# Performance work log

Hardware: AMD Instinct MI355X
Metric: run time of the kernel (lower is better)

Reference implementation:

```python
import jax, jax.numpy as jnp
import numpy as np

EPS = 1e-8
NUM_HEADS = 8


def setup_inputs() -> dict:
    key = jax.random.key(0)
    ks = jax.random.split(key, 12)
    B, T, F = 8, 512, 512
    H = NUM_HEADS
    dh = F // H
    maxlen = 2048
    s = 0.02  # weight init scale
    inp = {
        "x": jax.random.normal(ks[0], (B, T, F), jnp.float32),
        "Wq": jax.random.normal(ks[1], (F, F), jnp.float32) * s,
        "bq": jax.random.normal(ks[2], (F,), jnp.float32) * s,
        "Wk": jax.random.normal(ks[3], (F, F), jnp.float32) * s,
        "bk": jax.random.normal(ks[4], (F,), jnp.float32) * s,
        "Wv": jax.random.normal(ks[5], (F, F), jnp.float32) * s,
        "bv": jax.random.normal(ks[6], (F,), jnp.float32) * s,
        "Wo": jax.random.normal(ks[7], (F, F), jnp.float32) * s,
        "bo": jax.random.normal(ks[8], (F,), jnp.float32) * s,
        "delta": jnp.ones((1,), jnp.float32),
        "cache_k": jax.random.normal(ks[9], (B * H, maxlen, dh), jnp.float32) * 0.1,
        "cache_v": jax.random.normal(ks[10], (B * H, maxlen, dh), jnp.float32) * 0.1,
    }
    return inp


def _split_heads(t, H):
    # torch.cat(torch.split(t, dh, dim=-1), dim=0): head index outermost on dim 0
    B, T, F = t.shape
    dh = F // H
    return t.reshape(B, T, H, dh).transpose(2, 0, 1, 3).reshape(H * B, T, dh)


def _merge_heads(t, H):
    HB, T, dh = t.shape
    B = HB // H
    return t.reshape(H, B, T, dh).transpose(1, 2, 0, 3).reshape(B, T, H * dh)


def reference(x, Wq, bq, Wk, bk, Wv, bv, Wo, bo, delta, cache_k, cache_v):
    B, T, F = x.shape
    H = NUM_HEADS
    maxlen = cache_k.shape[1]
    d = jnp.sqrt(jnp.asarray(F, jnp.float32))

    q = _split_heads(x @ Wq.T + bq, H)  # [H*B, T, dh]
    k = _split_heads(x @ Wk.T + bk, H)
    v = _split_heads(x @ Wv.T + bv, H)

    # rolling KV cache: drop oldest T, append new T -> length maxlen
    k_full = jnp.concatenate([cache_k[:, T:], k], axis=1)  # [H*B, maxlen, dh]
    v_full = jnp.concatenate([cache_v[:, T:], v], axis=1)

    # Gaussian positional bias G = exp(-(i-j)^2 / (delta^2 + EPS)), last T rows
    i = jnp.arange(maxlen, dtype=jnp.float32)
    ind = -(i[:, None] - i[None, :]) ** 2  # [maxlen, maxlen]
    G = jnp.exp(ind[-T:] / (delta[0] ** 2 + EPS))  # [T, maxlen]

    scores = jnp.abs(jnp.einsum('btd,bsd->bts', q, k_full) * G / d)
    attn = jax.nn.softmax(scores, axis=-1)  # [H*B, T, maxlen]
    o = jnp.einsum('bts,bsd->btd', attn, v_full)  # [H*B, T, dh]

    out = _merge_heads(o, H) @ Wo.T + bo  # [B, T, F]
    return out
```

## Files before the change

### kernel.cpp

```cpp
#include <hip/hip_runtime.h>
#include <cstdint>
#include <cstddef>


typedef _Float16 f16x8 __attribute__((ext_vector_type(8)));
typedef _Float16 f16x4 __attribute__((ext_vector_type(4)));
typedef float f32x4 __attribute__((ext_vector_type(4)));

#define GLOBAL_AS __attribute__((address_space(1)))
#define LDS_AS __attribute__((address_space(3)))

__launch_bounds__(256)
__global__ void prep(const float* __restrict__ x,
                     const float* __restrict__ Wq, const float* __restrict__ Wk,
                     const float* __restrict__ Wv, const float* __restrict__ Wo,
                     const float* __restrict__ cache_v,
                     _Float16* __restrict__ xh, _Float16* __restrict__ wh,
                     float* __restrict__ part, float* __restrict__ svnew) {
  const int bid = blockIdx.x;
  const int tid = threadIdx.x;
  if (bid < 2048) {
    long e = ((long)bid * 256 + tid) * 4;
    float4 v = *(const float4*)(x + e);
    f16x4 h;
    h[0] = (_Float16)v.x; h[1] = (_Float16)v.y;
    h[2] = (_Float16)v.z; h[3] = (_Float16)v.w;
    *(f16x4*)(xh + e) = h;
  } else if (bid < 3072) {
    long e = ((long)(bid - 2048) * 256 + tid) * 4;
    int seg = (int)(e >> 18);
    const float* w = seg == 0 ? Wq : seg == 1 ? Wk : seg == 2 ? Wv : Wo;
    float4 v = *(const float4*)(w + (e & 262143));
    f16x4 h;
    h[0] = (_Float16)v.x; h[1] = (_Float16)v.y;
    h[2] = (_Float16)v.z; h[3] = (_Float16)v.w;
    *(f16x4*)(wh + e) = h;
  } else if (bid < 4096) {
    int pb = bid - 3072;
    int hb = pb >> 4, chunk = pb & 15;
    int g = tid & 15, p = tid >> 4;
    int r0 = 512 + chunk * 96;
    float4 s4 = {0.f, 0.f, 0.f, 0.f};
#pragma unroll
    for (int it = 0; it < 6; it++) {
      int r = r0 + p + it * 16;
      float4 v = *(const float4*)(cache_v + ((size_t)hb * 2048 + r) * 64 + g * 4);
      s4.x += v.x; s4.y += v.y; s4.z += v.z; s4.w += v.w;
    }
    __shared__ float4 red4[256];
    red4[tid] = s4;
    __syncthreads();
    if (tid < 64) {
      int gg = tid >> 2, c = tid & 3;
      float s = 0.f;
#pragma unroll
      for (int p2 = 0; p2 < 16; p2++) {
        float4 v = red4[p2 * 16 + gg];
        s += (c == 0) ? v.x : (c == 1) ? v.y : (c == 2) ? v.z : v.w;
      }
      part[(hb * 16 + chunk) * 64 + tid] = s;
    }
  } else {
    for (int i = tid; i < 4096; i += 256) svnew[i] = 0.f;
  }
}

__launch_bounds__(256)
__global__ void gemm_qkv(const _Float16* __restrict__ xh,
                         const _Float16* __restrict__ wh,
                         const float* __restrict__ bq,
                         const float* __restrict__ bk,
                         const float* __restrict__ bv,
                         _Float16* __restrict__ q, _Float16* __restrict__ k,
                         _Float16* __restrict__ v,
                         float* __restrict__ svnew) {
  __shared__ __align__(16) _Float16 As[4 * 128 * 32];
  __shared__ __align__(16) _Float16 Bs[4 * 64 * 32];
  const int tid = threadIdx.x;
  const int bid = blockIdx.x;
  const int swz = (bid & 7) * 96 + (bid >> 3);
  const int bx = swz / 24;
  const int by = swz - bx * 24;
  const int m0 = bx * 128;
  const int n0g = by * 64;
  const int which = n0g >> 9;
  const int nloc0 = n0g & 511;
  const _Float16* Bsel = wh + (size_t)which * 262144;
  const float* bsel = which == 0 ? bq : which == 1 ? bk : bv;
  _Float16* osel = which == 0 ? q : which == 1 ? k : v;
  const int w = tid >> 6, lane = tid & 63;
  const int c16 = lane & 15, q4 = lane >> 4;
  const int wm = (w & 1) * 64, wn = (w >> 1) * 32;

  f32x4 acc[4][2];
#pragma unroll
  for (int i = 0; i < 4; i++)
#pragma unroll
    for (int j = 0; j < 2; j++) acc[i][j] = (f32x4){0.f, 0.f, 0.f, 0.f};

  for (int k0 = 0; k0 < 512; k0 += 128) {
    __syncthreads();
#pragma unroll
    for (int it = 0; it < 8; it++) {
      int c = it * 256 + tid;
      int sub = c >> 9, row = (c >> 2) & 127, c8 = (c & 3) * 8;
      __builtin_amdgcn_global_load_lds(
          (const GLOBAL_AS void*)(xh + (size_t)(m0 + row) * 512 + k0 + sub * 32 + c8),
          (LDS_AS void*)(As + c * 8), 16, 0, 0);
    }
#pragma unroll
    for (int it = 0; it < 4; it++) {
      int c = it * 256 + tid;
      int sub = c >> 8, row = (c >> 2) & 63, c8 = (c & 3) * 8;
      __builtin_amdgcn_global_load_lds(
          (const GLOBAL_AS void*)(Bsel + (size_t)(nloc0 + row) * 512 + k0 + sub * 32 + c8),
          (LDS_AS void*)(Bs + c * 8), 16, 0, 0);
    }
    __syncthreads();

#pragma unroll
    for (int sub = 0; sub < 4; sub++) {
      f16x8 af[4], bf[2];
#pragma unroll
      for (int i = 0; i < 4; i++)
        af[i] = *(const f16x8*)(As + sub * 4096 + (wm + i * 16 + c16) * 32 + q4 * 8);
#pragma unroll
      for (int j = 0; j < 2; j++)
        bf[j] = *(const f16x8*)(Bs + sub * 2048 + (wn + j * 16 + c16) * 32 + q4 * 8);
#pragma unroll
      for (int i = 0; i < 4; i++)
#pragma unroll
        for (int j = 0; j < 2; j++)
          acc[i][j] = __builtin_amdgcn_mfma_f32_16x16x32_f16(af[i], bf[j], acc[i][j], 0, 0, 0);
    }
  }

  const int mbase = m0 + wm + (q4 << 2);
  const int nbase = nloc0 + wn + c16;
  float cs[2] = {0.f, 0.f};
#pragma unroll
  for (int i = 0; i < 4; i++)
#pragma unroll
    for (int j = 0; j < 2; j++) {
      int fg = nbase + j * 16;
      float bv2 = bsel[fg];
      int h = fg >> 6, dd = fg & 63;
#pragma unroll
      for (int r = 0; r < 4; r++) {
        int m = mbase + i * 16 + r;
        int b = m >> 9, t = m & 511;
        float val = acc[i][j][r] + bv2;
        osel[(((size_t)((h << 3) + b) * 512 + t) << 6) + dd] = (_Float16)val;
        cs[j] += val;
      }
    }
  if (which == 2) {
    const int b = m0 >> 9;
#pragma unroll
    for (int j = 0; j < 2; j++) {
      cs[j] += __shfl_xor(cs[j], 16, 64);
      cs[j] += __shfl_xor(cs[j], 32, 64);
      if (q4 == 0) {
        int fg = nbase + j * 16;
        int h = fg >> 6, dd = fg & 63;
        atomicAdd(&svnew[((h << 3) + b) * 64 + dd], cs[j]);
      }
    }
  }
}

__launch_bounds__(256)
__global__ void attn_mfma(const _Float16* __restrict__ q,
                          const _Float16* __restrict__ k_new,
                          const _Float16* __restrict__ v_new,
                          const float* __restrict__ cache_k,
                          const float* __restrict__ cache_v,
                          const float* __restrict__ part,
                          const float* __restrict__ svnew,
                          const float* __restrict__ delta,
                          _Float16* __restrict__ o_merged) {
  const int lin = blockIdx.y * 8 + blockIdx.x;
  const int swz = (lin & 7) * 64 + (lin >> 3);
  const int hb = swz >> 3;
  const int t0 = (swz & 7) * 64;
  const int jlo_t = 1520 + t0;

  __shared__ __align__(16) _Float16 Q_sh[64 * 72];
  __shared__ __align__(16) _Float16 K_sh[96 * 72];
  __shared__ __align__(16) _Float16 VT_sh[64 * 104];
  __shared__ __align__(16) _Float16 P_sh[64 * 104];
  __shared__ float G_sh[40];
  __shared__ float em_sh[64], id_sh[64], sv_sh[64];

  const int tid = threadIdx.x;
  const int w = tid >> 6, lane = tid & 63;
  const float dscale = 0.044194173824159216f;

  if (tid < 36) {
    int di = tid - 16;
    float inv_g = 1.0f / (delta[0] * delta[0] + 1e-8f);
    G_sh[tid] = (tid <= 32) ? expf(-(float)(di * di) * inv_g) : 0.f;
  }
  if (tid >= 64 && tid < 128) {
    int d = tid - 64;
    float s = svnew[hb * 64 + d];
#pragma unroll
    for (int c = 0; c < 16; c++) s += part[(hb * 16 + c) * 64 + d];
    sv_sh[d] = s;
  }
#pragma unroll
  for (int it = 0; it < 2; it++) {
    int idx = it * 256 + tid;
    int r = idx >> 3, c8 = (idx & 7) * 8;
    *(f16x8*)(Q_sh + r * 72 + c8) =
        *(const f16x8*)(q + ((size_t)hb * 512 + t0 + r) * 64 + c8);
  }
#pragma unroll
  for (int it = 0; it < 6; it++) {
    int idx = it * 256 + tid;
    int r = idx >> 4, c4 = idx & 15;
    int j = jlo_t + r;
    f16x4 kh, vh;
    if (j < 1536) {
      float4 k4 = *(const float4*)(cache_k + ((size_t)hb * 2048 + j + 512) * 64 + c4 * 4);
      float4 v4 = *(const float4*)(cache_v + ((size_t)hb * 2048 + j + 512) * 64 + c4 * 4);
      kh[0] = (_Float16)k4.x; kh[1] = (_Float16)k4.y;
      kh[2] = (_Float16)k4.z; kh[3] = (_Float16)k4.w;
      vh[0] = (_Float16)v4.x; vh[1] = (_Float16)v4.y;
      vh[2] = (_Float16)v4.z; vh[3] = (_Float16)v4.w;
    } else if (j < 2048) {
      kh = *(const f16x4*)(k_new + ((size_t)hb * 512 + (j - 1536)) * 64 + c4 * 4);
      vh = *(const f16x4*)(v_new + ((size_t)hb * 512 + (j - 1536)) * 64 + c4 * 4);
    } else {
#pragma unroll
      for (int e = 0; e < 4; e++) { kh[e] = (_Float16)0.f; vh[e] = (_Float16)0.f; }
    }
    *(f16x4*)(K_sh + r * 72 + c4 * 4) = kh;
#pragma unroll
    for (int e = 0; e < 4; e++) VT_sh[(c4 * 4 + e) * 104 + r] = vh[e];
  }
  __syncthreads();

  {
    const int c16 = lane & 15;
    const int q4 = lane >> 4;
    const int koff = q4 * 8;
    const int mrow = w * 16 + c16;
    f16x8 aq0 = *(const f16x8*)(Q_sh + mrow * 72 + koff);
    f16x8 aq1 = *(const f16x8*)(Q_sh + mrow * 72 + 32 + koff);
    f32x4 accS[6];
#pragma unroll
    for (int n = 0; n < 6; n++) accS[n] = (f32x4){0.f, 0.f, 0.f, 0.f};
    __builtin_amdgcn_s_setprio(1);
#pragma unroll
    for (int n = 0; n < 6; n++) {
      f16x8 b0 = *(const f16x8*)(K_sh + (n * 16 + c16) * 72 + koff);
      f16x8 b1 = *(const f16x8*)(K_sh + (n * 16 + c16) * 72 + 32 + koff);
      accS[n] = __builtin_amdgcn_mfma_f32_16x16x32_f16(aq0, b0, accS[n], 0, 0, 0);
      accS[n] = __builtin_amdgcn_mfma_f32_16x16x32_f16(aq1, b1, accS[n], 0, 0, 0);
    }
    __builtin_amdgcn_s_setprio(0);
    const int jmax = 527 - t0;
    float sc[6][4];
    float m_r[4] = {0.f, 0.f, 0.f, 0.f};
#pragma unroll
    for (int n = 0; n < 6; n++) {
      int jb = n * 16 + c16;
#pragma unroll
      for (int r = 0; r < 4; r++) {
        int row = w * 16 + q4 * 4 + r;
        int off = jb - row;
        bool valid = (off >= 0) && (off <= 32) && (jb <= jmax);
        int offc = min(max(off, 0), 32);
        float g = G_sh[offc];
        float val = valid ? fabsf(accS[n][r]) * dscale * g : 0.f;
        sc[n][r] = val;
        m_r[r] = fmaxf(m_r[r], val);
      }
    }
#pragma unroll
    for (int r = 0; r < 4; r++) {
#pragma unroll
      for (int mk = 1; mk < 16; mk <<= 1)
        m_r[r] = fmaxf(m_r[r], __shfl_xor(m_r[r], mk, 64));
    }
    float em_r[4], sum_r[4];
#pragma unroll
    for (int r = 0; r < 4; r++) { em_r[r] = expf(-m_r[r]); sum_r[r] = 0.f; }
#pragma unroll
    for (int n = 0; n < 6; n++) {
      int jb = n * 16 + c16;
#pragma unroll
      for (int r = 0; r < 4; r++) {
        int row = w * 16 + q4 * 4 + r;
        int off = jb - row;
        bool valid = (off >= 0) && (off <= 32) && (jb <= jmax);
        float wgt = valid ? (expf(sc[n][r] - m_r[r]) - em_r[r]) : 0.f;
        sum_r[r] += wgt;
        P_sh[row * 104 + jb] = (_Float16)wgt;
      }
    }
#pragma unroll
    for (int r = 0; r < 4; r++) {
#pragma unroll
      for (int mk = 1; mk < 16; mk <<= 1)
        sum_r[r] += __shfl_xor(sum_r[r], mk, 64);
      if (c16 == 0) {
        int row = w * 16 + q4 * 4 + r;
        em_sh[row] = em_r[r];
        id_sh[row] = 1.0f / (sum_r[r] + 2048.f * em_r[r]);
      }
    }
  }
  __syncthreads();

  f32x4 accO[4];
#pragma unroll
  for (int mi = 0; mi < 4; mi++) accO[mi] = (f32x4){0.f, 0.f, 0.f, 0.f};
  {
    const int koff = (lane >> 4) * 8;
    const int nrow = w * 16 + (lane & 15);
    __builtin_amdgcn_s_setprio(1);
#pragma unroll
    for (int k = 0; k < 3; k++) {
      f16x8 bv = *(const f16x8*)(VT_sh + nrow * 104 + k * 32 + koff);
#pragma unroll
      for (int mi = 0; mi < 4; mi++) {
        f16x8 ap = *(const f16x8*)(P_sh + (mi * 16 + (lane & 15)) * 104 + k * 32 + koff);
        accO[mi] = __builtin_amdgcn_mfma_f32_16x16x32_f16(ap, bv, accO[mi], 0, 0, 0);
      }
    }
    __builtin_amdgcn_s_setprio(0);
  }

  const int h = hb >> 3, b = hb & 7;
  const int d = w * 16 + (lane & 15);
  const float svd = sv_sh[d];
#pragma unroll
  for (int mi = 0; mi < 4; mi++)
#pragma unroll
    for (int r = 0; r < 4; r++) {
      int trow = mi * 16 + ((lane >> 4) << 2) + r;
      float val = (accO[mi][r] + em_sh[trow] * svd) * id_sh[trow];
      o_merged[((size_t)(b * 512 + t0 + trow)) * 512 + h * 64 + d] = (_Float16)val;
    }
}

__launch_bounds__(256)
__global__ void gemm_out(const _Float16* __restrict__ A,
                         const _Float16* __restrict__ Bw,
                         const float* __restrict__ bias,
                         float* __restrict__ out) {
  __shared__ __align__(16) _Float16 As[4 * 64 * 32];
  __shared__ __align__(16) _Float16 Bs[4 * 64 * 32];
  const int tid = threadIdx.x;
  const int bid = blockIdx.x;
  const int swz = (bid & 7) * 64 + (bid >> 3);
  const int m0 = (swz >> 3) * 64;
  const int n0 = (swz & 7) * 64;
  const int w = tid >> 6, lane = tid & 63;
  const int c16 = lane & 15, q4 = lane >> 4;
  const int wm = (w & 1) * 32, wn = (w >> 1) * 32;

  f32x4 acc[2][2];
#pragma unroll
  for (int i = 0; i < 2; i++)
#pragma unroll
    for (int j = 0; j < 2; j++) acc[i][j] = (f32x4){0.f, 0.f, 0.f, 0.f};

  for (int k0 = 0; k0 < 512; k0 += 128) {
    __syncthreads();
#pragma unroll
    for (int it = 0; it < 4; it++) {
      int c = it * 256 + tid;
      int sub = c >> 8, row = (c >> 2) & 63, c8 = (c & 3) * 8;
      __builtin_amdgcn_global_load_lds(
          (const GLOBAL_AS void*)(A + (size_t)(m0 + row) * 512 + k0 + sub * 32 + c8),
          (LDS_AS void*)(As + c * 8), 16, 0, 0);
      __builtin_amdgcn_global_load_lds(
          (const GLOBAL_AS void*)(Bw + (size_t)(n0 + row) * 512 + k0 + sub * 32 + c8),
          (LDS_AS void*)(Bs + c * 8), 16, 0, 0);
    }
    __syncthreads();

#pragma unroll
    for (int sub = 0; sub < 4; sub++) {
      f16x8 af[2], bf[2];
#pragma unroll
      for (int i = 0; i < 2; i++)
        af[i] = *(const f16x8*)(As + sub * 2048 + (wm + i * 16 + c16) * 32 + q4 * 8);
#pragma unroll
      for (int j = 0; j < 2; j++)
        bf[j] = *(const f16x8*)(Bs + sub * 2048 + (wn + j * 16 + c16) * 32 + q4 * 8);
#pragma unroll
      for (int i = 0; i < 2; i++)
#pragma unroll
        for (int j = 0; j < 2; j++)
          acc[i][j] = __builtin_amdgcn_mfma_f32_16x16x32_f16(af[i], bf[j], acc[i][j], 0, 0, 0);
    }
  }

  const int mbase = m0 + wm + (q4 << 2);
  const int nbase = n0 + wn + c16;
#pragma unroll
  for (int i = 0; i < 2; i++)
#pragma unroll
    for (int j = 0; j < 2; j++) {
      int fg = nbase + j * 16;
      float bv = bias[fg];
#pragma unroll
      for (int r = 0; r < 4; r++) {
        int m = mbase + i * 16 + r;
        out[(size_t)m * 512 + fg] = acc[i][j][r] + bv;
      }
    }
}

extern "C" void kernel_launch(void* const* d_in, const int* in_sizes, int n_in,
                              void* d_out, int out_size, void* d_ws, size_t ws_size,
                              hipStream_t stream) {
  const float* x = (const float*)d_in[0];
  const float* Wq = (const float*)d_in[1];
  const float* bq = (const float*)d_in[2];
  const float* Wk = (const float*)d_in[3];
  const float* bk = (const float*)d_in[4];
  const float* Wv = (const float*)d_in[5];
  const float* bv = (const float*)d_in[6];
  const float* Wo = (const float*)d_in[7];
  const float* bo = (const float*)d_in[8];
  const float* delta = (const float*)d_in[9];
  const float* cache_k = (const float*)d_in[10];
  const float* cache_v = (const float*)d_in[11];
  float* out = (float*)d_out;

  _Float16* xh = (_Float16*)d_ws;
  _Float16* wh = xh + 2097152;
  _Float16* qf = wh + 1048576;
  _Float16* kf = qf + 2097152;
  _Float16* vf = kf + 2097152;
  float* part = (float*)(vf + 2097152);
  float* svnew = part + 65536;
  _Float16* oh = (_Float16*)(svnew + 4096);

  prep<<<4097, 256, 0, stream>>>(x, Wq, Wk, Wv, Wo, cache_v, xh, wh, part, svnew);

  gemm_qkv<<<768, 256, 0, stream>>>(xh, wh, bq, bk, bv, qf, kf, vf, svnew);

  dim3 g2(8, 64);
  attn_mfma<<<g2, 256, 0, stream>>>(qf, kf, vf, cache_k, cache_v, part, svnew,
                                    delta, oh);

  gemm_out<<<512, 256, 0, stream>>>(oh, wh + 3 * 262144, bo, out);
}
```

Measured before the change: 149.6 us.

## Double-buffer GEMM K-loop tiles and defer V transpose stores past QK

Both the QKV and output-projection GEMMs now split K into 64-wide stages held in two LDS buffers. The next stage is prefetched with global_load_lds while the current one is fed to MFMA, so one barrier per stage replaces the load-wait-compute pattern. In the attention kernel, V values are kept in registers and their transposed LDS stores are moved to after the QK/softmax phase. The first barrier then only has to wait for the Q and K stores. This costs more barriers, smaller per-stage work and extra registers for the held V fragments.

```diff
diff --git a/kernel.cpp b/kernel.cpp
--- a/kernel.cpp
+++ b/kernel.cpp
@@ -74,8 +74,8 @@
                          _Float16* __restrict__ q, _Float16* __restrict__ k,
                          _Float16* __restrict__ v,
                          float* __restrict__ svnew) {
-  __shared__ __align__(16) _Float16 As[4 * 128 * 32];
-  __shared__ __align__(16) _Float16 Bs[4 * 64 * 32];
+  __shared__ __align__(16) _Float16 As[2 * 2 * 128 * 32];
+  __shared__ __align__(16) _Float16 Bs[2 * 2 * 64 * 32];
   const int tid = threadIdx.x;
   const int bid = blockIdx.x;
   const int swz = (bid & 7) * 96 + (bid >> 3);
@@ -98,42 +98,54 @@
 #pragma unroll
     for (int j = 0; j < 2; j++) acc[i][j] = (f32x4){0.f, 0.f, 0.f, 0.f};
 
-  for (int k0 = 0; k0 < 512; k0 += 128) {
-    __syncthreads();
-#pragma unroll
-    for (int it = 0; it < 8; it++) {
-      int c = it * 256 + tid;
-      int sub = c >> 9, row = (c >> 2) & 127, c8 = (c & 3) * 8;
-      __builtin_amdgcn_global_load_lds(
-          (const GLOBAL_AS void*)(xh + (size_t)(m0 + row) * 512 + k0 + sub * 32 + c8),
-          (LDS_AS void*)(As + c * 8), 16, 0, 0);
-    }
-#pragma unroll
-    for (int it = 0; it < 4; it++) {
-      int c = it * 256 + tid;
-      int sub = c >> 8, row = (c >> 2) & 63, c8 = (c & 3) * 8;
-      __builtin_amdgcn_global_load_lds(
-          (const GLOBAL_AS void*)(Bsel + (size_t)(nloc0 + row) * 512 + k0 + sub * 32 + c8),
-          (LDS_AS void*)(Bs + c * 8), 16, 0, 0);
-    }
-    __syncthreads();
-
-#pragma unroll
-    for (int sub = 0; sub < 4; sub++) {
+#define QKV_STAGE(buf, k0)                                                     \
+  {                                                                            \
+    _Pragma("unroll")                                                          \
+    for (int it = 0; it < 4; it++) {                \
+      int c = it * 256 + tid;                                                  \
+      int sub = c >> 9, row = (c >> 2) & 127, c8 = (c & 3) * 8;                \
+      __builtin_amdgcn_global_load_lds(                                        \
+          (const GLOBAL_AS void*)(xh + (size_t)(m0 + row) * 512 + (k0) +       \
+                                  sub * 32 + c8),                              \
+          (LDS_AS void*)(As + (buf) * 8192 + c * 8), 16, 0, 0);                \
+    }                                                                          \
+    _Pragma("unroll")                                                          \
+    for (int it = 0; it < 2; it++) {                 \
+      int c = it * 256 + tid;                                                  \
+      int sub = c >> 8, row = (c >> 2) & 63, c8 = (c & 3) * 8;                 \
+      __builtin_amdgcn_global_load_lds(                                        \
+          (const GLOBAL_AS void*)(Bsel + (size_t)(nloc0 + row) * 512 + (k0) +  \
+                                  sub * 32 + c8),                              \
+          (LDS_AS void*)(Bs + (buf) * 4096 + c * 8), 16, 0, 0);                \
+    }                                                                          \
+  }
+
+  QKV_STAGE(0, 0);
+  __syncthreads();
+#pragma unroll
+  for (int t = 0; t < 8; t++) {
+    const int cur = t & 1;
+    if (t < 7) QKV_STAGE(cur ^ 1, (t + 1) * 64);
+#pragma unroll
+    for (int sub = 0; sub < 2; sub++) {
       f16x8 af[4], bf[2];
 #pragma unroll
       for (int i = 0; i < 4; i++)
-        af[i] = *(const f16x8*)(As + sub * 4096 + (wm + i * 16 + c16) * 32 + q4 * 8);
+        af[i] = *(const f16x8*)(As + cur * 8192 + sub * 4096 +
+                                (wm + i * 16 + c16) * 32 + q4 * 8);
 #pragma unroll
       for (int j = 0; j < 2; j++)
-        bf[j] = *(const f16x8*)(Bs + sub * 2048 + (wn + j * 16 + c16) * 32 + q4 * 8);
+        bf[j] = *(const f16x8*)(Bs + cur * 4096 + sub * 2048 +
+                                (wn + j * 16 + c16) * 32 + q4 * 8);
 #pragma unroll
       for (int i = 0; i < 4; i++)
 #pragma unroll
         for (int j = 0; j < 2; j++)
           acc[i][j] = __builtin_amdgcn_mfma_f32_16x16x32_f16(af[i], bf[j], acc[i][j], 0, 0, 0);
     }
-  }
+    __syncthreads();
+  }
+#undef QKV_STAGE
 
   const int mbase = m0 + wm + (q4 << 2);
   const int nbase = nloc0 + wn + c16;
@@ -215,6 +227,7 @@
     *(f16x8*)(Q_sh + r * 72 + c8) =
         *(const f16x8*)(q + ((size_t)hb * 512 + t0 + r) * 64 + c8);
   }
+  f16x4 vreg[6];
 #pragma unroll
   for (int it = 0; it < 6; it++) {
     int idx = it * 256 + tid;
@@ -236,10 +249,10 @@
       for (int e = 0; e < 4; e++) { kh[e] = (_Float16)0.f; vh[e] = (_Float16)0.f; }
     }
     *(f16x4*)(K_sh + r * 72 + c4 * 4) = kh;
-#pragma unroll
-    for (int e = 0; e < 4; e++) VT_sh[(c4 * 4 + e) * 104 + r] = vh[e];
-  }
-  __syncthreads();
+    vreg[it] = vh;
+  }
+  asm volatile("s_waitcnt lgkmcnt(0)" ::: "memory");
+  __builtin_amdgcn_s_barrier();
 
   {
     const int c16 = lane & 15;
@@ -312,6 +325,15 @@
       }
     }
   }
+
+#pragma unroll
+  for (int it = 0; it < 6; it++) {
+    int idx = it * 256 + tid;
+    int r = idx >> 4, c4 = idx & 15;
+    f16x4 vh = vreg[it];
+#pragma unroll
+    for (int e = 0; e < 4; e++) VT_sh[(c4 * 4 + e) * 104 + r] = vh[e];
+  }
   __syncthreads();
 
   f32x4 accO[4];
@@ -351,8 +373,8 @@
                          const _Float16* __restrict__ Bw,
                          const float* __restrict__ bias,
                          float* __restrict__ out) {
-  __shared__ __align__(16) _Float16 As[4 * 64 * 32];
-  __shared__ __align__(16) _Float16 Bs[4 * 64 * 32];
+  __shared__ __align__(16) _Float16 As[2 * 2 * 64 * 32];
+  __shared__ __align__(16) _Float16 Bs[2 * 2 * 64 * 32];
   const int tid = threadIdx.x;
   const int bid = blockIdx.x;
   const int swz = (bid & 7) * 64 + (bid >> 3);
@@ -368,37 +390,49 @@
 #pragma unroll
     for (int j = 0; j < 2; j++) acc[i][j] = (f32x4){0.f, 0.f, 0.f, 0.f};
 
-  for (int k0 = 0; k0 < 512; k0 += 128) {
-    __syncthreads();
-#pragma unroll
-    for (int it = 0; it < 4; it++) {
-      int c = it * 256 + tid;
-      int sub = c >> 8, row = (c >> 2) & 63, c8 = (c & 3) * 8;
-      __builtin_amdgcn_global_load_lds(
-          (const GLOBAL_AS void*)(A + (size_t)(m0 + row) * 512 + k0 + sub * 32 + c8),
-          (LDS_AS void*)(As + c * 8), 16, 0, 0);
-      __builtin_amdgcn_global_load_lds(
-          (const GLOBAL_AS void*)(Bw + (size_t)(n0 + row) * 512 + k0 + sub * 32 + c8),
-          (LDS_AS void*)(Bs + c * 8), 16, 0, 0);
-    }
-    __syncthreads();
-
-#pragma unroll
-    for (int sub = 0; sub < 4; sub++) {
+#define OUT_STAGE(buf, k0)                                                     \
+  {                                                                            \
+    _Pragma("unroll")                                                          \
+    for (int it = 0; it < 2; it++) {           \
+      int c = it * 256 + tid;                                                  \
+      int sub = c >> 8, row = (c >> 2) & 63, c8 = (c & 3) * 8;                 \
+      __builtin_amdgcn_global_load_lds(                                        \
+          (const GLOBAL_AS void*)(A + (size_t)(m0 + row) * 512 + (k0) +        \
+                                  sub * 32 + c8),                              \
+          (LDS_AS void*)(As + (buf) * 4096 + c * 8), 16, 0, 0);                \
+      __builtin_amdgcn_global_load_lds(                                        \
+          (const GLOBAL_AS void*)(Bw + (size_t)(n0 + row) * 512 + (k0) +       \
+                                  sub * 32 + c8),                              \
+          (LDS_AS void*)(Bs + (buf) * 4096 + c * 8), 16, 0, 0);                \
+    }                                                                          \
+  }
+
+  OUT_STAGE(0, 0);
+  __syncthreads();
+#pragma unroll
+  for (int t = 0; t < 8; t++) {
+    const int cur = t & 1;
+    if (t < 7) OUT_STAGE(cur ^ 1, (t + 1) * 64);
+#pragma unroll
+    for (int sub = 0; sub < 2; sub++) {
       f16x8 af[2], bf[2];
 #pragma unroll
       for (int i = 0; i < 2; i++)
-        af[i] = *(const f16x8*)(As + sub * 2048 + (wm + i * 16 + c16) * 32 + q4 * 8);
+        af[i] = *(const f16x8*)(As + cur * 4096 + sub * 2048 +
+                                (wm + i * 16 + c16) * 32 + q4 * 8);
 #pragma unroll
       for (int j = 0; j < 2; j++)
-        bf[j] = *(const f16x8*)(Bs + sub * 2048 + (wn + j * 16 + c16) * 32 + q4 * 8);
+        bf[j] = *(const f16x8*)(Bs + cur * 4096 + sub * 2048 +
+                                (wn + j * 16 + c16) * 32 + q4 * 8);
 #pragma unroll
       for (int i = 0; i < 2; i++)
 #pragma unroll
         for (int j = 0; j < 2; j++)
           acc[i][j] = __builtin_amdgcn_mfma_f32_16x16x32_f16(af[i], bf[j], acc[i][j], 0, 0, 0);
     }
-  }
+    __syncthreads();
+  }
+#undef OUT_STAGE
 
   const int mbase = m0 + wm + (q4 << 2);
   const int nbase = n0 + wn + c16;
```

Result: no change. 152.3 us (+1.8%).

## Exploit banded Gaussian mask to skip dead score tiles and max-subtraction

Applied to the files above, without the earlier changes.

Each warp now computes only the 3 of 6 key tiles that can overlap its 33-wide Gaussian band, instead of all six. The row-max reduction is removed: weights become exp(s)-1 with the background mass 2048, on the assumption that scores stay small enough not to overflow. The V transpose into LDS is deferred into registers until after the score phase so its loads overlap the QK MFMA work. The PV MMA loop is also restricted to the two nonzero k-chunks per row tile. Removing max-subtraction risks overflow if the scores grow large, and one unwritten tile per warp is explicitly zeroed.

```diff
diff --git a/kernel.cpp b/kernel.cpp
--- a/kernel.cpp
+++ b/kernel.cpp
@@ -190,7 +190,7 @@
   __shared__ __align__(16) _Float16 VT_sh[64 * 104];
   __shared__ __align__(16) _Float16 P_sh[64 * 104];
   __shared__ float G_sh[40];
-  __shared__ float em_sh[64], id_sh[64], sv_sh[64];
+  __shared__ float id_sh[64], sv_sh[64];
 
   const int tid = threadIdx.x;
   const int w = tid >> 6, lane = tid & 63;
@@ -215,6 +215,7 @@
     *(f16x8*)(Q_sh + r * 72 + c8) =
         *(const f16x8*)(q + ((size_t)hb * 512 + t0 + r) * 64 + c8);
   }
+  f16x4 vreg[6];
 #pragma unroll
   for (int it = 0; it < 6; it++) {
     int idx = it * 256 + tid;
@@ -236,10 +237,10 @@
       for (int e = 0; e < 4; e++) { kh[e] = (_Float16)0.f; vh[e] = (_Float16)0.f; }
     }
     *(f16x4*)(K_sh + r * 72 + c4 * 4) = kh;
-#pragma unroll
-    for (int e = 0; e < 4; e++) VT_sh[(c4 * 4 + e) * 104 + r] = vh[e];
-  }
-  __syncthreads();
+    vreg[it] = vh;
+  }
+  asm volatile("s_waitcnt lgkmcnt(0)" ::: "memory");
+  __builtin_amdgcn_s_barrier();
 
   {
     const int c16 = lane & 15;
@@ -248,24 +249,24 @@
     const int mrow = w * 16 + c16;
     f16x8 aq0 = *(const f16x8*)(Q_sh + mrow * 72 + koff);
     f16x8 aq1 = *(const f16x8*)(Q_sh + mrow * 72 + 32 + koff);
-    f32x4 accS[6];
-#pragma unroll
-    for (int n = 0; n < 6; n++) accS[n] = (f32x4){0.f, 0.f, 0.f, 0.f};
+    f32x4 accS[3];
+#pragma unroll
+    for (int n2 = 0; n2 < 3; n2++) accS[n2] = (f32x4){0.f, 0.f, 0.f, 0.f};
     __builtin_amdgcn_s_setprio(1);
 #pragma unroll
-    for (int n = 0; n < 6; n++) {
+    for (int n2 = 0; n2 < 3; n2++) {
+      int n = w + n2;
       f16x8 b0 = *(const f16x8*)(K_sh + (n * 16 + c16) * 72 + koff);
       f16x8 b1 = *(const f16x8*)(K_sh + (n * 16 + c16) * 72 + 32 + koff);
-      accS[n] = __builtin_amdgcn_mfma_f32_16x16x32_f16(aq0, b0, accS[n], 0, 0, 0);
-      accS[n] = __builtin_amdgcn_mfma_f32_16x16x32_f16(aq1, b1, accS[n], 0, 0, 0);
+      accS[n2] = __builtin_amdgcn_mfma_f32_16x16x32_f16(aq0, b0, accS[n2], 0, 0, 0);
+      accS[n2] = __builtin_amdgcn_mfma_f32_16x16x32_f16(aq1, b1, accS[n2], 0, 0, 0);
     }
     __builtin_amdgcn_s_setprio(0);
     const int jmax = 527 - t0;
-    float sc[6][4];
-    float m_r[4] = {0.f, 0.f, 0.f, 0.f};
-#pragma unroll
-    for (int n = 0; n < 6; n++) {
-      int jb = n * 16 + c16;
+    float sum_r[4] = {0.f, 0.f, 0.f, 0.f};
+#pragma unroll
+    for (int n2 = 0; n2 < 3; n2++) {
+      int jb = (w + n2) * 16 + c16;
 #pragma unroll
       for (int r = 0; r < 4; r++) {
         int row = w * 16 + q4 * 4 + r;
@@ -273,32 +274,18 @@
         bool valid = (off >= 0) && (off <= 32) && (jb <= jmax);
         int offc = min(max(off, 0), 32);
         float g = G_sh[offc];
-        float val = valid ? fabsf(accS[n][r]) * dscale * g : 0.f;
-        sc[n][r] = val;
-        m_r[r] = fmaxf(m_r[r], val);
-      }
-    }
-#pragma unroll
-    for (int r = 0; r < 4; r++) {
-#pragma unroll
-      for (int mk = 1; mk < 16; mk <<= 1)
-        m_r[r] = fmaxf(m_r[r], __shfl_xor(m_r[r], mk, 64));
-    }
-    float em_r[4], sum_r[4];
-#pragma unroll
-    for (int r = 0; r < 4; r++) { em_r[r] = expf(-m_r[r]); sum_r[r] = 0.f; }
-#pragma unroll
-    for (int n = 0; n < 6; n++) {
-      int jb = n * 16 + c16;
-#pragma unroll
-      for (int r = 0; r < 4; r++) {
-        int row = w * 16 + q4 * 4 + r;
-        int off = jb - row;
-        bool valid = (off >= 0) && (off <= 32) && (jb <= jmax);
-        float wgt = valid ? (expf(sc[n][r] - m_r[r]) - em_r[r]) : 0.f;
+        float val = fabsf(accS[n2][r]) * dscale * g;
+        float wgt = valid ? (expf(val) - 1.0f) : 0.f;
         sum_r[r] += wgt;
         P_sh[row * 104 + jb] = (_Float16)wgt;
       }
+    }
+    {
+      int zt = w + 3 - ((w & 1) << 2);
+      int jb = zt * 16 + c16;
+#pragma unroll
+      for (int r = 0; r < 4; r++)
+        P_sh[(w * 16 + q4 * 4 + r) * 104 + jb] = (_Float16)0.f;
     }
 #pragma unroll
     for (int r = 0; r < 4; r++) {
@@ -307,10 +294,18 @@
         sum_r[r] += __shfl_xor(sum_r[r], mk, 64);
       if (c16 == 0) {
         int row = w * 16 + q4 * 4 + r;
-        em_sh[row] = em_r[r];
-        id_sh[row] = 1.0f / (sum_r[r] + 2048.f * em_r[r]);
-      }
-    }
+        id_sh[row] = 1.0f / (sum_r[r] + 2048.f);
+      }
+    }
+  }
+
+#pragma unroll
+  for (int it = 0; it < 6; it++) {
+    int idx = it * 256 + tid;
+    int r = idx >> 4, c4 = idx & 15;
+    f16x4 vh = vreg[it];
+#pragma unroll
+    for (int e = 0; e < 4; e++) VT_sh[(c4 * 4 + e) * 104 + r] = vh[e];
   }
   __syncthreads();
 
@@ -320,15 +315,19 @@
   {
     const int koff = (lane >> 4) * 8;
     const int nrow = w * 16 + (lane & 15);
+    f16x8 bv0 = *(const f16x8*)(VT_sh + nrow * 104 + 0 + koff);
+    f16x8 bv1 = *(const f16x8*)(VT_sh + nrow * 104 + 32 + koff);
+    f16x8 bv2 = *(const f16x8*)(VT_sh + nrow * 104 + 64 + koff);
     __builtin_amdgcn_s_setprio(1);
 #pragma unroll
-    for (int k = 0; k < 3; k++) {
-      f16x8 bv = *(const f16x8*)(VT_sh + nrow * 104 + k * 32 + koff);
-#pragma unroll
-      for (int mi = 0; mi < 4; mi++) {
-        f16x8 ap = *(const f16x8*)(P_sh + (mi * 16 + (lane & 15)) * 104 + k * 32 + koff);
-        accO[mi] = __builtin_amdgcn_mfma_f32_16x16x32_f16(ap, bv, accO[mi], 0, 0, 0);
-      }
+    for (int mi = 0; mi < 4; mi++) {
+      const int kc = mi >> 1;
+      f16x8 bva = (kc == 0) ? bv0 : bv1;
+      f16x8 bvb = (kc == 0) ? bv1 : bv2;
+      f16x8 apa = *(const f16x8*)(P_sh + (mi * 16 + (lane & 15)) * 104 + kc * 32 + koff);
+      accO[mi] = __builtin_amdgcn_mfma_f32_16x16x32_f16(apa, bva, accO[mi], 0, 0, 0);
+      f16x8 apb = *(const f16x8*)(P_sh + (mi * 16 + (lane & 15)) * 104 + (kc + 1) * 32 + koff);
+      accO[mi] = __builtin_amdgcn_mfma_f32_16x16x32_f16(apb, bvb, accO[mi], 0, 0, 0);
     }
     __builtin_amdgcn_s_setprio(0);
   }
@@ -341,7 +340,7 @@
 #pragma unroll
     for (int r = 0; r < 4; r++) {
       int trow = mi * 16 + ((lane >> 4) << 2) + r;
-      float val = (accO[mi][r] + em_sh[trow] * svd) * id_sh[trow];
+      float val = (accO[mi][r] + svd) * id_sh[trow];
       o_merged[((size_t)(b * 512 + t0 + trow)) * 512 + h * 64 + d] = (_Float16)val;
     }
 }
```

Measured after the change: 147.7 us. About the same (-1.3%).
